# Kernel tuning notes

Hardware: AMD Instinct MI355X
Metric: run time of the kernel (lower is better)

Reference implementation:

```python
import jax, jax.numpy as jnp
import numpy as np

B, T, H = 16, 64, 256  # batch, timesteps (= num stacked layers), hidden
L = T                  # MultiRNNCell([cell]*timesteps): layers == timesteps, shared weights


def setup_inputs() -> dict:
    key = jax.random.key(0)
    k1, k2, k3 = jax.random.split(key, 3)
    x = jax.random.normal(k1, (B, T, H), dtype=jnp.float32)
    init_state = jax.random.normal(k2, (L, 2, B, H), dtype=jnp.float32) * 0.1  # [L, (c,h), B, H]
    W = jax.random.normal(k3, (2 * H, 4 * H), dtype=jnp.float32) / np.sqrt(2 * H)
    b = jnp.zeros((4 * H,), dtype=jnp.float32)
    return {"x": x, "init_state": init_state, "W": W, "b": b}


def reference(x, init_state, W, b):
    # TF LSTMCell math: gates order (i, j, f, o), forget_bias = 1.0
    c0 = init_state[:, 0]  # [L,B,H]
    h0 = init_state[:, 1]  # [L,B,H]

    def layer_fn(inp, st):
        # inp: [B,H] input to this layer; st = (c,h) each [B,H]
        lc, lh = st
        z = jnp.concatenate([inp, lh], axis=-1) @ W + b  # [B,4H]
        i, j, f, o = jnp.split(z, 4, axis=-1)
        nc = jax.nn.sigmoid(f + 1.0) * lc + jax.nn.sigmoid(i) * jnp.tanh(j)
        nh = jax.nn.sigmoid(o) * jnp.tanh(nc)
        return nh, (nc, nh)  # carry = input to next layer; ys = new per-layer state

    def step(carry, xt):
        # carry: (c,h) each [L,B,H]; xt: [B,H]
        c, h = carry
        top_h, (nc, nh) = jax.lax.scan(layer_fn, xt, (c, h))
        return (nc, nh), top_h

    (_, _), ys = jax.lax.scan(step, (c0, h0), jnp.transpose(x, (1, 0, 2)))  # ys: [T,B,H]
    return jnp.transpose(ys, (1, 0, 2))  # [B,T,H] top-layer outputs (dynamic_rnn outputs)
```

## Files before the change

### kernel.cpp

```cpp
#include <hip/hip_runtime.h>

typedef _Float16 half8 __attribute__((ext_vector_type(8)));
typedef float f32x4 __attribute__((ext_vector_type(4)));
typedef unsigned int u32;
typedef unsigned int u32x4 __attribute__((ext_vector_type(4)));

#define SC_AGENT __HIP_MEMORY_SCOPE_AGENT

constexpr size_t OFF_PROG  = 0;
constexpr size_t OFF_EPOCH = 4096;
constexpr size_t OFF_H     = 65536;
constexpr size_t S4 = (size_t)64 * 16 * 256;

__device__ __forceinline__ float sigm(float v) { return 1.0f / (1.0f + __expf(-v)); }
__device__ __forceinline__ float tanh_(float v) { return 1.0f - 2.0f / (__expf(2.0f * v) + 1.0f); }

#define GLD4(dst, base, OFS)                                                  \
  asm volatile("global_load_dwordx4 %0, %1, off offset:" #OFS " sc0 sc1"      \
               : "=v"(dst) : "v"(base))

__global__ void bump_epoch(char* ws) {
  u32* ep = (u32*)(ws + OFF_EPOCH);
  u32 v = __hip_atomic_load(ep, __ATOMIC_RELAXED, SC_AGENT);
  u32 n = (v + 1) & 0x1FFu;
  if (n == 0) n = 1;
  __hip_atomic_store(ep, n, __ATOMIC_RELAXED, SC_AGENT);
}

__global__ void init_ws(const float* __restrict__ init_state, char* ws) {
  u32* prog = (u32*)(ws + OFF_PROG);
  u32* Hw4 = (u32*)(ws + OFF_H);
  const u32 ep = __hip_atomic_load((u32*)(ws + OFF_EPOCH), __ATOMIC_RELAXED, SC_AGENT);
  const u32 epb = (ep & 0x1FFu) << 7;
  const int tid = blockIdx.x * 256 + threadIdx.x;
  if (tid < 256) prog[tid] = epb - 1u;
  const u32 tagInit = (epb | 127u) << 16;
  for (int e = tid; e < 64 * 16 * 256; e += 65536) {
    const int u = e & 255, b = (e >> 8) & 15, l = e >> 12;
    const size_t idx = ((size_t)l * 16 + b) * 256 + u;
    Hw4[idx] = 0u;
    union { _Float16 f; unsigned short s; } hv;
    hv.f = (_Float16)init_state[((l * 2 + 1) * 16 + b) * 256 + u];
    Hw4[S4 + idx] = (u32)hv.s | tagInit;
  }
}

__global__ __launch_bounds__(256, 1) void lstm_mfma(
    const float* __restrict__ x, const float* __restrict__ init_state,
    const float* __restrict__ W, const float* __restrict__ bias,
    float* __restrict__ out, char* ws) {
  u32* prog = (u32*)(ws + OFF_PROG);
  u32* Hw4 = (u32*)(ws + OFF_H);

  const int tid = threadIdx.x;
  const int wg = blockIdx.x;
  const int l = wg >> 2, r = wg & 3;
  const int wv = tid >> 6, lane = tid & 63;

  const u32 epb = (__hip_atomic_load((u32*)(ws + OFF_EPOCH), __ATOMIC_RELAXED,
                                     SC_AGENT) & 0x1FFu) << 7;

  __shared__ alignas(16) _Float16 aLds[16 * 64 * 8];

  half8 wreg[64];
#pragma unroll
  for (int q = 0; q < 4; ++q) {
    const int nl = (wv * 4 + q) * 16 + (lane & 15);
    const int col = (nl & 3) * 256 + r * 64 + (nl >> 2);
#pragma unroll
    for (int kb = 0; kb < 16; ++kb) {
      const int k0 = kb * 32 + (lane >> 4) * 8;
      const float* src = W + (size_t)k0 * 1024 + col;
      half8 hv;
#pragma unroll
      for (int jj = 0; jj < 8; ++jj) hv[jj] = (_Float16)src[(size_t)jj * 1024];
      wreg[q * 16 + kb] = hv;
    }
  }

  const int m_own = (lane >> 4) * 4 + (lane & 3);
  int gu_q[4];
  float creg[4], bI[4], bJ[4], bF[4], bO[4];
#pragma unroll
  for (int q = 0; q < 4; ++q) {
    const int u_q = (wv * 4 + q) * 4 + ((lane & 15) >> 2);
    gu_q[q] = r * 64 + u_q;
    creg[q] = init_state[((l * 2 + 0) * 16 + m_own) * 256 + gu_q[q]];
    bI[q] = bias[0 * 256 + gu_q[q]];
    bJ[q] = bias[1 * 256 + gu_q[q]];
    bF[q] = bias[2 * 256 + gu_q[q]];
    bO[q] = bias[3 * 256 + gu_q[q]];
  }

  const int m = lane & 15;
  const int ksub = (lane >> 4) * 8;

  u32 plCache = 0, bpCache = 0;

  for (int t = 0; t < 64; ++t) {
    const int slotCur = t & 1, slotPrev = (t + 1) & 1;
    const u32 expIn = epb | (u32)t;
    const u32 expOwn = (t > 0) ? (epb | (u32)(t - 1)) : (epb | 127u);

    if (l == 0) {
#pragma unroll
      for (int i = 0; i < 2; ++i) {
        const int kb = i * 4 + wv;
        const int k0 = kb * 32 + ksub;
        const float* xs = x + ((size_t)m * 64 + t) * 256 + k0;
        half8 hv;
#pragma unroll
        for (int jj = 0; jj < 8; ++jj) hv[jj] = (_Float16)xs[jj];
        *(half8*)&aLds[(size_t)(kb * 64 + lane) * 8] = hv;
      }
    }

    if (l > 0 && plCache < (epb | (u32)t)) {
      u32* pb = &prog[(l - 1) * 4];
      int g = 0;
      while (true) {
        u32x4 pv;
        GLD4(pv, pb, 0);
        asm volatile("s_waitcnt vmcnt(0)" ::: "memory");
        __builtin_amdgcn_sched_barrier(0);
        u32 mn = pv[0] < pv[1] ? pv[0] : pv[1];
        mn = mn < pv[2] ? mn : pv[2];
        mn = mn < pv[3] ? mn : pv[3];
        plCache = mn;
        if (mn >= (epb | (u32)t)) break;
        __builtin_amdgcn_s_sleep(4);
        if (++g > 800000) break;
      }
    }

    if (tid == 0 && l < 63 && t >= 2 && bpCache < (epb | (u32)(t - 2))) {
      u32* pb = &prog[(l + 1) * 4];
      int g = 0;
      while (true) {
        u32x4 pv;
        GLD4(pv, pb, 0);
        asm volatile("s_waitcnt vmcnt(0)" ::: "memory");
        __builtin_amdgcn_sched_barrier(0);
        u32 mn = pv[0] < pv[1] ? pv[0] : pv[1];
        mn = mn < pv[2] ? mn : pv[2];
        mn = mn < pv[3] ? mn : pv[3];
        bpCache = mn;
        if (mn >= (epb | (u32)(t - 2))) break;
        __builtin_amdgcn_s_sleep(2);
        if (++g > 800000) break;
      }
    }

    unsigned pend = (l == 0) ? 0xF0u : 0xFFu;
    const u32* pLow = Hw4 + (slotCur ? S4 : 0) +
                      (((size_t)(l > 0 ? l - 1 : 0) * 16 + m) * 256) + wv * 32 + ksub;
    const u32* pHigh = Hw4 + (slotPrev ? S4 : 0) +
                       (((size_t)l * 16 + m) * 256) + wv * 32 + ksub;
    int round = 0;
    while (pend) {
      u32x4 gv[8];
      if (pend & 0x01u) GLD4(gv[0], pLow, 0);
      if (pend & 0x02u) GLD4(gv[1], pLow, 16);
      if (pend & 0x04u) GLD4(gv[2], pLow, 512);
      if (pend & 0x08u) GLD4(gv[3], pLow, 528);
      if (pend & 0x10u) GLD4(gv[4], pHigh, 0);
      if (pend & 0x20u) GLD4(gv[5], pHigh, 16);
      if (pend & 0x40u) GLD4(gv[6], pHigh, 512);
      if (pend & 0x80u) GLD4(gv[7], pHigh, 528);
      asm volatile("s_waitcnt vmcnt(0)" ::: "memory");
      __builtin_amdgcn_sched_barrier(0);
#pragma unroll
      for (int b = 0; b < 8; ++b) {
        if ((pend >> b) & 1u) {
          const u32 exp_ = (b < 4) ? expIn : expOwn;
          const u32x4 v = gv[b];
          if ((v[0] >> 16) == exp_ && (v[1] >> 16) == exp_ &&
              (v[2] >> 16) == exp_ && (v[3] >> 16) == exp_) {
            const int kb = (b >> 1) * 4 + wv;
            u32* dp = (u32*)&aLds[(size_t)(kb * 64 + lane) * 8 + (b & 1) * 4];
            dp[0] = (v[0] & 0xFFFFu) | (v[1] << 16);
            dp[1] = (v[2] & 0xFFFFu) | (v[3] << 16);
            pend &= ~(1u << b);
          }
        }
      }
      if (pend) {
        if (++round > 500000) break;
        if (round > 32 && (round & 3) == 0) __builtin_amdgcn_s_sleep(1);
      }
    }
    __syncthreads();
    if (tid == 0)
      __hip_atomic_store(&prog[l * 4 + r], epb | (u32)t, __ATOMIC_RELAXED, SC_AGENT);

    f32x4 acc[4] = {{0.f, 0.f, 0.f, 0.f}, {0.f, 0.f, 0.f, 0.f},
                    {0.f, 0.f, 0.f, 0.f}, {0.f, 0.f, 0.f, 0.f}};
#pragma unroll
    for (int kb = 0; kb < 16; ++kb) {
      half8 a = *(const half8*)&aLds[(kb * 64 + lane) * 8];
#pragma unroll
      for (int q = 0; q < 4; ++q)
        acc[q] = __builtin_amdgcn_mfma_f32_16x16x32_f16(a, wreg[q * 16 + kb], acc[q], 0, 0, 0);
    }
    __syncthreads();

#pragma unroll
    for (int q = 0; q < 4; ++q) {
      float v0 = acc[q][0], v1 = acc[q][1], v2 = acc[q][2], v3 = acc[q][3];
      float e0 = __shfl_xor(v1, 1, 64), e1 = __shfl_xor(v0, 1, 64);
      float e2 = __shfl_xor(v3, 1, 64), e3 = __shfl_xor(v2, 1, 64);
      const bool o1 = (lane & 1);
      float m0 = o1 ? e0 : v0, m1 = o1 ? v1 : e1;
      float m2 = o1 ? e2 : v2, m3 = o1 ? v3 : e3;
      float f0 = __shfl_xor(m2, 2, 64), f1 = __shfl_xor(m3, 2, 64);
      float f2 = __shfl_xor(m0, 2, 64), f3 = __shfl_xor(m1, 2, 64);
      const bool o2 = (lane & 2);
      float gI = o2 ? f0 : m0, gJ = o2 ? f1 : m1;
      float gF = o2 ? m2 : f2, gO = o2 ? m3 : f3;

      const float iv = gI + bI[q], jv = gJ + bJ[q];
      const float fv = gF + bF[q], ov = gO + bO[q];
      const float nc = sigm(fv + 1.0f) * creg[q] + sigm(iv) * tanh_(jv);
      const float nh = sigm(ov) * tanh_(nc);
      creg[q] = nc;
      union { _Float16 f; unsigned short s; } cv;
      cv.f = (_Float16)nh;
      const size_t idx = (slotCur ? S4 : 0) +
                         ((size_t)l * 16 + m_own) * 256 + gu_q[q];
      __hip_atomic_store(Hw4 + idx, (u32)cv.s | (expIn << 16),
                         __ATOMIC_RELAXED, SC_AGENT);
      if (l == 63) out[((size_t)m_own * 64 + t) * 256 + gu_q[q]] = nh;
    }
  }
}

extern "C" void kernel_launch(void* const* d_in, const int* in_sizes, int n_in,
                              void* d_out, int out_size, void* d_ws,
                              size_t ws_size, hipStream_t stream) {
  const float* x          = (const float*)d_in[0];
  const float* init_state = (const float*)d_in[1];
  const float* W          = (const float*)d_in[2];
  const float* bias       = (const float*)d_in[3];
  float* out = (float*)d_out;
  char* ws   = (char*)d_ws;

  bump_epoch<<<1, 1, 0, stream>>>(ws);
  init_ws<<<256, 256, 0, stream>>>(init_state, ws);
  lstm_mfma<<<256, 256, 0, stream>>>(x, init_state, W, bias, out, ws);
}
```

Baseline: 677.1 us.

## Merge progress polling into data wait loop and keep own h slice in LDS

```diff
diff --git a/kernel.cpp b/kernel.cpp
--- a/kernel.cpp
+++ b/kernel.cpp
@@ -14,6 +14,11 @@
 
 __device__ __forceinline__ float sigm(float v) { return 1.0f / (1.0f + __expf(-v)); }
 __device__ __forceinline__ float tanh_(float v) { return 1.0f - 2.0f / (__expf(2.0f * v) + 1.0f); }
+__device__ __forceinline__ u32 min4(u32x4 v) {
+  u32 a = v[0] < v[1] ? v[0] : v[1];
+  u32 b = v[2] < v[3] ? v[2] : v[3];
+  return a < b ? a : b;
+}
 
 #define GLD4(dst, base, OFS)                                                  \
   asm volatile("global_load_dwordx4 %0, %1, off offset:" #OFS " sc0 sc1"      \
@@ -92,10 +97,22 @@
     bO[q] = bias[3 * 256 + gu_q[q]];
   }
 
+#pragma unroll
+  for (int q = 0; q < 4; ++q) {
+    const int gu = gu_q[q];
+    const float h0 = init_state[((l * 2 + 1) * 16 + m_own) * 256 + gu];
+    aLds[(size_t)((8 + (gu >> 5)) * 64 + ((((gu & 31) >> 3) << 4) | m_own)) * 8 +
+         (gu & 7)] = (_Float16)h0;
+  }
+
   const int m = lane & 15;
   const int ksub = (lane >> 4) * 8;
+  const u32 ownMask = ((wv >> 1) == r) ? 0x30u
+                    : (((wv + 4) >> 1) == r) ? 0xC0u : 0u;
 
   u32 plCache = 0, bpCache = 0;
+  u32* const plBase = &prog[(l > 0 ? l - 1 : 0) * 4];
+  u32* const bpBase = &prog[(l < 63 ? l + 1 : 63) * 4];
 
   for (int t = 0; t < 64; ++t) {
     const int slotCur = t & 1, slotPrev = (t + 1) & 1;
@@ -115,78 +132,59 @@
       }
     }
 
-    if (l > 0 && plCache < (epb | (u32)t)) {
-      u32* pb = &prog[(l - 1) * 4];
-      int g = 0;
-      while (true) {
-        u32x4 pv;
-        GLD4(pv, pb, 0);
-        asm volatile("s_waitcnt vmcnt(0)" ::: "memory");
-        __builtin_amdgcn_sched_barrier(0);
-        u32 mn = pv[0] < pv[1] ? pv[0] : pv[1];
-        mn = mn < pv[2] ? mn : pv[2];
-        mn = mn < pv[3] ? mn : pv[3];
-        plCache = mn;
-        if (mn >= (epb | (u32)t)) break;
-        __builtin_amdgcn_s_sleep(4);
-        if (++g > 800000) break;
-      }
-    }
-
-    if (tid == 0 && l < 63 && t >= 2 && bpCache < (epb | (u32)(t - 2))) {
-      u32* pb = &prog[(l + 1) * 4];
-      int g = 0;
-      while (true) {
-        u32x4 pv;
-        GLD4(pv, pb, 0);
-        asm volatile("s_waitcnt vmcnt(0)" ::: "memory");
-        __builtin_amdgcn_sched_barrier(0);
-        u32 mn = pv[0] < pv[1] ? pv[0] : pv[1];
-        mn = mn < pv[2] ? mn : pv[2];
-        mn = mn < pv[3] ? mn : pv[3];
-        bpCache = mn;
-        if (mn >= (epb | (u32)(t - 2))) break;
-        __builtin_amdgcn_s_sleep(2);
-        if (++g > 800000) break;
-      }
-    }
-
-    unsigned pend = (l == 0) ? 0xF0u : 0xFFu;
+    unsigned pend = ((l == 0) ? 0xF0u : 0xFFu) & ~ownMask;
+    const bool bpNeed = (tid == 0 && l < 63 && t >= 2);
+    bool bpOK = !bpNeed || bpCache >= (epb | (u32)(t - 2));
     const u32* pLow = Hw4 + (slotCur ? S4 : 0) +
                       (((size_t)(l > 0 ? l - 1 : 0) * 16 + m) * 256) + wv * 32 + ksub;
     const u32* pHigh = Hw4 + (slotPrev ? S4 : 0) +
                        (((size_t)l * 16 + m) * 256) + wv * 32 + ksub;
     int round = 0;
-    while (pend) {
-      u32x4 gv[8];
-      if (pend & 0x01u) GLD4(gv[0], pLow, 0);
-      if (pend & 0x02u) GLD4(gv[1], pLow, 16);
-      if (pend & 0x04u) GLD4(gv[2], pLow, 512);
-      if (pend & 0x08u) GLD4(gv[3], pLow, 528);
-      if (pend & 0x10u) GLD4(gv[4], pHigh, 0);
-      if (pend & 0x20u) GLD4(gv[5], pHigh, 16);
-      if (pend & 0x40u) GLD4(gv[6], pHigh, 512);
-      if (pend & 0x80u) GLD4(gv[7], pHigh, 528);
+    while (pend || !bpOK) {
+      const bool ready = (l == 0) || (plCache >= (epb | (u32)t));
+      const bool didData = ready && pend;
+      u32x4 gv[8], pv, bv;
+      if (didData) {
+        if (pend & 0x01u) GLD4(gv[0], pLow, 0);
+        if (pend & 0x02u) GLD4(gv[1], pLow, 16);
+        if (pend & 0x04u) GLD4(gv[2], pLow, 512);
+        if (pend & 0x08u) GLD4(gv[3], pLow, 528);
+        if (pend & 0x10u) GLD4(gv[4], pHigh, 0);
+        if (pend & 0x20u) GLD4(gv[5], pHigh, 16);
+        if (pend & 0x40u) GLD4(gv[6], pHigh, 512);
+        if (pend & 0x80u) GLD4(gv[7], pHigh, 528);
+      }
+      const bool didGate = (l > 0) && !ready;
+      if (didGate) GLD4(pv, plBase, 0);
+      if (!bpOK) GLD4(bv, bpBase, 0);
       asm volatile("s_waitcnt vmcnt(0)" ::: "memory");
       __builtin_amdgcn_sched_barrier(0);
-#pragma unroll
-      for (int b = 0; b < 8; ++b) {
-        if ((pend >> b) & 1u) {
-          const u32 exp_ = (b < 4) ? expIn : expOwn;
-          const u32x4 v = gv[b];
-          if ((v[0] >> 16) == exp_ && (v[1] >> 16) == exp_ &&
-              (v[2] >> 16) == exp_ && (v[3] >> 16) == exp_) {
-            const int kb = (b >> 1) * 4 + wv;
-            u32* dp = (u32*)&aLds[(size_t)(kb * 64 + lane) * 8 + (b & 1) * 4];
-            dp[0] = (v[0] & 0xFFFFu) | (v[1] << 16);
-            dp[1] = (v[2] & 0xFFFFu) | (v[3] << 16);
-            pend &= ~(1u << b);
+      if (didGate) plCache = min4(pv);
+      if (!bpOK) {
+        bpCache = min4(bv);
+        bpOK = bpCache >= (epb | (u32)(t - 2));
+      }
+      if (didData) {
+#pragma unroll
+        for (int b = 0; b < 8; ++b) {
+          if ((pend >> b) & 1u) {
+            const u32 exp_ = (b < 4) ? expIn : expOwn;
+            const u32x4 v = gv[b];
+            if ((v[0] >> 16) == exp_ && (v[1] >> 16) == exp_ &&
+                (v[2] >> 16) == exp_ && (v[3] >> 16) == exp_) {
+              const int kb = (b >> 1) * 4 + wv;
+              u32* dp = (u32*)&aLds[(size_t)(kb * 64 + lane) * 8 + (b & 1) * 4];
+              dp[0] = (v[0] & 0xFFFFu) | (v[1] << 16);
+              dp[1] = (v[2] & 0xFFFFu) | (v[3] << 16);
+              pend &= ~(1u << b);
+            }
           }
         }
       }
-      if (pend) {
+      if (pend || !bpOK) {
         if (++round > 500000) break;
-        if (round > 32 && (round & 3) == 0) __builtin_amdgcn_s_sleep(1);
+        if (!ready) __builtin_amdgcn_s_sleep(4);
+        else if (round > 64 && (round & 3) == 0) __builtin_amdgcn_s_sleep(1);
       }
     }
     __syncthreads();
@@ -225,11 +223,14 @@
       creg[q] = nc;
       union { _Float16 f; unsigned short s; } cv;
       cv.f = (_Float16)nh;
+      const int gu = gu_q[q];
       const size_t idx = (slotCur ? S4 : 0) +
-                         ((size_t)l * 16 + m_own) * 256 + gu_q[q];
+                         ((size_t)l * 16 + m_own) * 256 + gu;
       __hip_atomic_store(Hw4 + idx, (u32)cv.s | (expIn << 16),
                          __ATOMIC_RELAXED, SC_AGENT);
-      if (l == 63) out[((size_t)m_own * 64 + t) * 256 + gu_q[q]] = nh;
+      aLds[(size_t)((8 + (gu >> 5)) * 64 + ((((gu & 31) >> 3) << 4) | m_own)) * 8 +
+           (gu & 7)] = cv.f;
+      if (l == 63) out[((size_t)m_own * 64 + t) * 256 + gu] = nh;
     }
   }
 }
```

New measurement: 686.0 us. No clear change (+1.3%).
